# Kernel optimization log

Measured on AMD Instinct MI355X. Metric: run time of the kernel, lower is better.

Reference implementation:

```python
import jax, jax.numpy as jnp
import numpy as np
from jax import lax

N_QUBITS = 8
N_LAYERS = 7


def _conv(x, w, b, stride, pad):
    y = lax.conv_general_dilated(x, w, (stride, stride), [(pad, pad), (pad, pad)],
                                 dimension_numbers=('NCHW', 'OIHW', 'NCHW'))
    return y + b[None, :, None, None]


def _apply_1q(psi, M, q):
    # psi: (B, 2,2,...,2); apply 2x2 real matrix M on qubit q (axis q+1)
    a = q + 1
    pm = jnp.moveaxis(psi, a, 1)
    out = jnp.einsum('ij,bj...->bi...', M, pm)
    return jnp.moveaxis(out, 1, a)


def _apply_cnot(psi, c, t):
    ac, at = c + 1, t + 1
    pm = jnp.moveaxis(psi, (ac, at), (1, 2))
    top = pm[:, 0]
    bot = jnp.flip(pm[:, 1], axis=1)  # flip target when control=1
    pm = jnp.stack([top, bot], axis=1)
    return jnp.moveaxis(pm, (1, 2), (ac, at))


def _quantum(features, qw):
    psi = features / jnp.linalg.norm(features, axis=1, keepdims=True)
    B = psi.shape[0]
    psi = psi.reshape((B,) + (2,) * N_QUBITS)
    for l in range(N_LAYERS):
        for q in range(N_QUBITS):
            th = qw[l, q] / 2.0
            c, s = jnp.cos(th), jnp.sin(th)
            M = jnp.stack([jnp.stack([c, -s]), jnp.stack([s, c])])
            psi = _apply_1q(psi, M, q)
        for q in range(N_QUBITS - 1):
            psi = _apply_cnot(psi, q, q + 1)
    p = psi.reshape(B, 2, -1) ** 2
    return jnp.sum(p[:, 0], axis=1) - jnp.sum(p[:, 1], axis=1)  # <PauliZ(0)>


def setup_inputs() -> dict:
    key = jax.random.key(0)
    ks = jax.random.split(key, 20)
    def g(k, shape, fan_in):
        return jax.random.normal(k, shape, jnp.float32) * (1.0 / np.sqrt(fan_in))
    inp = {
        'x':  jax.random.normal(ks[0], (4096, 1, 64, 64), jnp.float32),
        'w1': g(ks[1], (4, 1, 5, 5), 25), 'b1': jnp.zeros((4,), jnp.float32),
        'w2': g(ks[2], (8, 4, 3, 3), 36), 'b2': jnp.zeros((8,), jnp.float32),
        'w3': g(ks[3], (16, 8, 3, 3), 72), 'b3': jnp.zeros((16,), jnp.float32),
        'wf': g(ks[4], (256, 64), 64), 'bf': jnp.zeros((256,), jnp.float32),
        'qw': jax.random.uniform(ks[5], (7, 8), jnp.float32, 0.0, 2 * np.pi),
        'wc1': g(ks[6], (200, 1), 1),   'bc1': jnp.zeros((200,), jnp.float32),
        'wc2': g(ks[7], (150, 200), 200), 'bc2': jnp.zeros((150,), jnp.float32),
        'wc3': g(ks[8], (100, 150), 150), 'bc3': jnp.zeros((100,), jnp.float32),
        'wc4': g(ks[9], (50, 100), 100),  'bc4': jnp.zeros((50,), jnp.float32),
        'wc5': g(ks[10], (1, 50), 50),    'bc5': jnp.zeros((1,), jnp.float32),
    }
    return inp


def reference(x, w1, b1, w2, b2, w3, b3, wf, bf, qw,
              wc1, bc1, wc2, bc2, wc3, bc3, wc4, bc4, wc5, bc5):
    # CNN feature extractor (dropout = identity at inference)
    h = jax.nn.relu(_conv(x, w1, b1, 2, 2))   # (B,4,32,32)
    h = jax.nn.relu(_conv(h, w2, b2, 2, 1))   # (B,8,16,16)
    h = jax.nn.relu(_conv(h, w3, b3, 1, 1))   # (B,16,16,16)
    B = h.shape[0]
    # AdaptiveAvgPool2d(2): 16x16 -> 2x2 via 8x8 non-overlapping means
    h = h.reshape(B, 16, 2, 8, 2, 8).mean(axis=(3, 5))  # (B,16,2,2)
    h = h.reshape(B, 64)
    feats = jax.nn.relu(h @ wf.T + bf)        # (B,256)
    # F.normalize(p=2, dim=1)
    feats = feats / jnp.maximum(jnp.linalg.norm(feats, axis=1, keepdims=True), 1e-12)
    # Batched 8-qubit statevector simulation (replaces per-sample Python loop)
    q = _quantum(feats, qw)[:, None]          # (B,1)
    # MLP classifier
    h = jax.nn.relu(q @ wc1.T + bc1)
    h = jax.nn.relu(h @ wc2.T + bc2)
    h = jax.nn.relu(h @ wc3.T + bc3)
    h = jax.nn.relu(h @ wc4.T + bc4)
    return jax.nn.sigmoid(h @ wc5.T + bc5)    # (B,1)
```

## Files before the change

### kernel.cpp

```cpp
#include <hip/hip_runtime.h>
#include <math.h>

typedef float v2f __attribute__((ext_vector_type(2)));
#define FMA2(a, b, c) __builtin_elementwise_fma((a), (b), (c))

__global__ __launch_bounds__(256, 8)
void convpool_kernel(const float* __restrict__ x,
                     const float* __restrict__ w1, const float* __restrict__ b1,
                     const float* __restrict__ w2, const float* __restrict__ b2,
                     const float* __restrict__ w3, const float* __restrict__ b3,
                     float* __restrict__ poolout)
{
    __shared__ __align__(16) float arena[4648];
    const int tid  = threadIdx.x;
    const int b    = blockIdx.x;
    const int lane = tid & 63;

    float wstage[7];
    #pragma unroll
    for (int j = 0; j < 7; j++) {
        const int s  = tid + 256 * j;
        const int oc = s / 100;
        const int r  = s - oc * 100;
        const int ic = r / 12;
        const int k  = r - ic * 12;
        wstage[j] = (s < 1600 && r < 96 && k < 9) ? w3[oc * 72 + ic * 9 + k] : 0.f;
    }
    const float bstage = (tid < 16) ? b3[tid] : 0.f;

    if (tid < 40) arena[4608 + tid] = 0.f;

    {
        const float* xb = x + (size_t)b * 4096;
        const int oh  = tid >> 3;
        const int ow  = tid & 7;
        const int ow0 = ow * 4;
        const int c0  = ow0 * 2 - 2;
        const bool cmL = (ow == 0);
        const bool cmR = (ow == 7);
        v2f a01[4], a23[4];
        #pragma unroll
        for (int oc = 0; oc < 4; oc++) {
            const float bv = b1[oc];
            a01[oc] = (v2f){bv, bv};
            a23[oc] = (v2f){bv, bv};
        }
        #pragma unroll
        for (int kh = 0; kh < 5; kh++) {
            const int ih = oh * 2 - 2 + kh;
            if (ih >= 0 && ih < 64) {
                const float* row = xb + ih * 64;
                float colv[11];
                {
                    float v0 = row[cmL ? 0 : c0];
                    float v1 = row[cmL ? 0 : c0 + 1];
                    float vA = row[cmR ? 63 : c0 + 10];
                    colv[0]  = cmL ? 0.f : v0;
                    colv[1]  = cmL ? 0.f : v1;
                    colv[10] = cmR ? 0.f : vA;
                }
                {
                    const float4 m0 = *(const float4*)(row + c0 + 2);
                    const float4 m1 = *(const float4*)(row + c0 + 6);
                    colv[2] = m0.x; colv[3] = m0.y; colv[4] = m0.z; colv[5] = m0.w;
                    colv[6] = m1.x; colv[7] = m1.y; colv[8] = m1.z; colv[9] = m1.w;
                }
                #pragma unroll
                for (int kw = 0; kw < 5; kw++) {
                    const v2f c01 = {colv[kw],     colv[kw + 2]};
                    const v2f c23 = {colv[kw + 4], colv[kw + 6]};
                    #pragma unroll
                    for (int oc = 0; oc < 4; oc++) {
                        const float wv = w1[oc * 25 + kh * 5 + kw];
                        const v2f ws = {wv, wv};
                        a01[oc] = FMA2(c01, ws, a01[oc]);
                        a23[oc] = FMA2(c23, ws, a23[oc]);
                    }
                }
            }
        }
        const int bsw1 = (oh >> 1) & 1;
        #pragma unroll
        for (int oc = 0; oc < 4; oc++) {
            float4 v;
            v.x = fmaxf(a01[oc].x, 0.f); v.y = fmaxf(a01[oc].y, 0.f);
            v.z = fmaxf(a23[oc].x, 0.f); v.w = fmaxf(a23[oc].y, 0.f);
            *(float4*)(arena + oc * 1152 + oh * 36 + ((ow ^ bsw1) << 2)) = v;
        }
    }
    __syncthreads();

    v2f rA01, rA23, rB01, rB23;
    {
        const int oc0 = __builtin_amdgcn_readfirstlane(tid >> 6);
        const int oh  = lane >> 2;
        const int w   = lane & 3;
        {
            const float ba = b2[oc0], bb = b2[oc0 + 4];
            rA01 = (v2f){ba, ba}; rA23 = (v2f){ba, ba};
            rB01 = (v2f){bb, bb}; rB23 = (v2f){bb, bb};
        }
        #pragma unroll
        for (int ic = 0; ic < 4; ic++) {
            const float* base = arena + ic * 1152;
            #pragma unroll
            for (int kh = 0; kh < 3; kh++) {
                const int r2 = 2 * oh + kh - 1;
                const bool zr = (kh == 0) && (oh == 0);
                const int rc = zr ? 0 : r2;
                const int bsw = (rc >> 1) & 1;
                const float* row = zr ? (arena + 4608) : (base + rc * 36);
                const float4 qA = *(const float4*)(row + (((2 * w)     ^ bsw) << 2));
                const float4 qB = *(const float4*)(row + (((2 * w + 1) ^ bsw) << 2));
                const int sblk = (w == 0) ? bsw : ((2 * w - 1) ^ bsw);
                const float sv = row[(sblk << 2) + 3];
                float colv[9];
                colv[0] = (w == 0) ? 0.f : sv;
                colv[1] = qA.x; colv[2] = qA.y; colv[3] = qA.z; colv[4] = qA.w;
                colv[5] = qB.x; colv[6] = qB.y; colv[7] = qB.z; colv[8] = qB.w;
                #pragma unroll
                for (int kw = 0; kw < 3; kw++) {
                    const v2f c01 = {colv[kw],     colv[kw + 2]};
                    const v2f c23 = {colv[kw + 4], colv[kw + 6]};
                    const float wa = w2[((oc0    ) * 4 + ic) * 9 + kh * 3 + kw];
                    const float wb = w2[((oc0 + 4) * 4 + ic) * 9 + kh * 3 + kw];
                    const v2f was = {wa, wa}, wbs = {wb, wb};
                    rA01 = FMA2(c01, was, rA01);
                    rA23 = FMA2(c23, was, rA23);
                    rB01 = FMA2(c01, wbs, rB01);
                    rB23 = FMA2(c23, wbs, rB23);
                }
            }
        }
    }
    __syncthreads();

    for (int i = tid; i < 544; i += 256) {
        const int ch = i / 68, j = i - ch * 68;
        if (j < 18)      arena[ch * 360 + j] = 0.f;
        else if (j < 36) arena[ch * 360 + 17 * 20 + (j - 18)] = 0.f;
        else if (j < 52) arena[ch * 360 + (j - 35) * 20] = 0.f;
        else             arena[ch * 360 + (j - 51) * 20 + 17] = 0.f;
    }
    {
        const int oc0 = __builtin_amdgcn_readfirstlane(tid >> 6);
        const int oh  = lane >> 2, ow0 = (lane & 3) * 4;
        float* oA = arena + oc0 * 360       + (oh + 1) * 20 + ow0 + 1;
        float* oB = arena + (oc0 + 4) * 360 + (oh + 1) * 20 + ow0 + 1;
        oA[0] = fmaxf(rA01.x, 0.f); oA[1] = fmaxf(rA01.y, 0.f);
        oA[2] = fmaxf(rA23.x, 0.f); oA[3] = fmaxf(rA23.y, 0.f);
        oB[0] = fmaxf(rB01.x, 0.f); oB[1] = fmaxf(rB01.y, 0.f);
        oB[2] = fmaxf(rB23.x, 0.f); oB[3] = fmaxf(rB23.y, 0.f);
    }
    #pragma unroll
    for (int j = 0; j < 7; j++) {
        const int s = tid + 256 * j;
        if (s < 1600) arena[2880 + s] = wstage[j];
    }
    if (tid < 16) arena[4480 + tid] = bstage;
    __syncthreads();

    {
        const float* w3s = arena + 2880;
        const int oc = tid >> 4, s = tid & 15;
        const int tr = (s >> 2) * 4, tc = (s & 3) * 4;
        v2f acc2[4][2];
        const float bv = w3s[1600 + oc];
        #pragma unroll
        for (int r = 0; r < 4; r++) {
            acc2[r][0] = (v2f){bv, bv};
            acc2[r][1] = (v2f){bv, bv};
        }
        #pragma unroll
        for (int ic = 0; ic < 8; ic++) {
            const float* xc = arena + ic * 360;
            const float4 wv0 = *(const float4*)(w3s + oc * 100 + ic * 12);
            const float4 wv1 = *(const float4*)(w3s + oc * 100 + ic * 12 + 4);
            const float  wv8 = w3s[oc * 100 + ic * 12 + 8];
            const float wv[9] = {wv0.x, wv0.y, wv0.z, wv0.w, wv1.x, wv1.y, wv1.z, wv1.w, wv8};
            #pragma unroll
            for (int j = 0; j < 6; j++) {
                const float* rp = xc + (tr + j) * 20 + tc;
                const float4 qa = *(const float4*)(rp);
                const float4 qb = *(const float4*)(rp + 4);
                const v2f e0 = {qa.x, qa.y};
                const v2f o0 = {qa.y, qa.z};
                const v2f e1 = {qa.z, qa.w};
                const v2f o1 = {qa.w, qb.x};
                const v2f e2 = {qb.x, qb.y};
                #pragma unroll
                for (int r = 0; r < 4; r++) {
                    const int kh = j - r;
                    if (kh >= 0 && kh < 3) {
                        const v2f w0s = {wv[kh * 3 + 0], wv[kh * 3 + 0]};
                        const v2f w1s = {wv[kh * 3 + 1], wv[kh * 3 + 1]};
                        const v2f w2s = {wv[kh * 3 + 2], wv[kh * 3 + 2]};
                        acc2[r][0] = FMA2(e0, w0s, acc2[r][0]);
                        acc2[r][0] = FMA2(o0, w1s, acc2[r][0]);
                        acc2[r][0] = FMA2(e1, w2s, acc2[r][0]);
                        acc2[r][1] = FMA2(e1, w0s, acc2[r][1]);
                        acc2[r][1] = FMA2(o1, w1s, acc2[r][1]);
                        acc2[r][1] = FMA2(e2, w2s, acc2[r][1]);
                    }
                }
            }
        }
        float ps = 0.f;
        #pragma unroll
        for (int r = 0; r < 4; r++) {
            ps += fmaxf(acc2[r][0].x, 0.f);
            ps += fmaxf(acc2[r][0].y, 0.f);
            ps += fmaxf(acc2[r][1].x, 0.f);
            ps += fmaxf(acc2[r][1].y, 0.f);
        }
        ps += __shfl_xor(ps, 1, 64);
        ps += __shfl_xor(ps, 4, 64);
        if ((s & 5) == 0) {
            const int ii = s >> 3, jj = (s >> 1) & 1;
            poolout[b * 64 + oc * 4 + ii * 2 + jj] = ps * (1.f / 64.f);
        }
    }
}

__global__ __launch_bounds__(256)
void head_kernel(const float* __restrict__ poolin,
                 const float* __restrict__ wf, const float* __restrict__ bf,
                 const float* __restrict__ qw,
                 const float* __restrict__ wc1, const float* __restrict__ bc1,
                 const float* __restrict__ wc2, const float* __restrict__ bc2,
                 const float* __restrict__ wc3, const float* __restrict__ bc3,
                 const float* __restrict__ wc4, const float* __restrict__ bc4,
                 const float* __restrict__ wc5, const float* __restrict__ bc5,
                 float* __restrict__ out)
{
    __shared__ __align__(16) float pool_s[256];
    __shared__ __align__(16) float feats[1024];
    __shared__ __align__(16) float h1[800];
    __shared__ __align__(16) float h2[600];
    __shared__ __align__(16) float h3[400];
    __shared__ __align__(16) float h4[200];
    __shared__ float zbuf[4];
    __shared__ float csc[56], css[56];

    const int tid  = threadIdx.x;
    const int blk  = blockIdx.x;
    const int lane = tid & 63;
    const int wv   = tid >> 6;

    pool_s[tid] = poolin[(size_t)blk * 256 + tid];
    if (tid < 56) {
        float th = qw[tid] * 0.5f;
        csc[tid] = cosf(th);
        css[tid] = sinf(th);
    }
    __syncthreads();

    {
        float acc[4];
        const float bv = bf[tid];
        #pragma unroll
        for (int e = 0; e < 4; e++) acc[e] = bv;
        const float4* wr = (const float4*)(wf + tid * 64);
        #pragma unroll
        for (int kc = 0; kc < 4; kc++) {
            float4 w0 = wr[kc * 4 + 0], w1_ = wr[kc * 4 + 1], w2_ = wr[kc * 4 + 2], w3_ = wr[kc * 4 + 3];
            #pragma unroll
            for (int e = 0; e < 4; e++) {
                const float4* pp = (const float4*)(pool_s + e * 64 + kc * 16);
                float4 p0 = pp[0], p1 = pp[1], p2 = pp[2], p3 = pp[3];
                float a = acc[e];
                a = fmaf(w0.x, p0.x, a); a = fmaf(w0.y, p0.y, a); a = fmaf(w0.z, p0.z, a); a = fmaf(w0.w, p0.w, a);
                a = fmaf(w1_.x, p1.x, a); a = fmaf(w1_.y, p1.y, a); a = fmaf(w1_.z, p1.z, a); a = fmaf(w1_.w, p1.w, a);
                a = fmaf(w2_.x, p2.x, a); a = fmaf(w2_.y, p2.y, a); a = fmaf(w2_.z, p2.z, a); a = fmaf(w2_.w, p2.w, a);
                a = fmaf(w3_.x, p3.x, a); a = fmaf(w3_.y, p3.y, a); a = fmaf(w3_.z, p3.z, a); a = fmaf(w3_.w, p3.w, a);
                acc[e] = a;
            }
        }
        #pragma unroll
        for (int e = 0; e < 4; e++) feats[e * 256 + tid] = fmaxf(acc[e], 0.f);
    }
    __syncthreads();

    {
        const float* base = feats + wv * 256;
        float v0 = base[lane], v1 = base[64 + lane];
        float v2 = base[128 + lane], v3 = base[192 + lane];
        float ssq = v0 * v0 + v1 * v1 + v2 * v2 + v3 * v3;
        #pragma unroll
        for (int off = 1; off < 64; off <<= 1) ssq += __shfl_xor(ssq, off, 64);
        const float inv = 1.0f / fmaxf(sqrtf(ssq), 1e-12f);
        v0 *= inv; v1 *= inv; v2 *= inv; v3 *= inv;

        for (int l = 0; l < 7; l++) {
            {
                float c = csc[l * 8 + 0], s = css[l * 8 + 0];
                float n0 = c * v0 - s * v2, n2 = s * v0 + c * v2;
                float n1 = c * v1 - s * v3, n3 = s * v1 + c * v3;
                float c1 = csc[l * 8 + 1], s1 = css[l * 8 + 1];
                v0 = c1 * n0 - s1 * n1; v1 = s1 * n0 + c1 * n1;
                v2 = c1 * n2 - s1 * n3; v3 = s1 * n2 + c1 * n3;
            }
            #pragma unroll
            for (int q = 2; q < 8; q++) {
                const int m = 1 << (7 - q);
                const float c = csc[l * 8 + q], s = css[l * 8 + q];
                const float sgn = (lane & m) ? s : -s;
                float t0 = __shfl_xor(v0, m, 64);
                float t1 = __shfl_xor(v1, m, 64);
                float t2 = __shfl_xor(v2, m, 64);
                float t3 = __shfl_xor(v3, m, 64);
                v0 = fmaf(sgn, t0, c * v0);
                v1 = fmaf(sgn, t1, c * v1);
                v2 = fmaf(sgn, t2, c * v2);
                v3 = fmaf(sgn, t3, c * v3);
            }
            { float t = v2; v2 = v3; v3 = t; }
            v1 = __shfl_xor(v1, 32, 64);
            v3 = __shfl_xor(v3, 32, 64);
            #pragma unroll
            for (int q = 2; q < 7; q++) {
                const int mc = 1 << (7 - q), mt = 1 << (6 - q);
                float t0 = __shfl_xor(v0, mt, 64);
                float t1 = __shfl_xor(v1, mt, 64);
                float t2 = __shfl_xor(v2, mt, 64);
                float t3 = __shfl_xor(v3, mt, 64);
                if (lane & mc) { v0 = t0; v1 = t1; v2 = t2; v3 = t3; }
            }
        }
        float m0 = v0 * v0 + v1 * v1 - v2 * v2 - v3 * v3;
        #pragma unroll
        for (int off = 1; off < 64; off <<= 1) m0 += __shfl_xor(m0, off, 64);
        if (lane == 0) zbuf[wv] = m0;
    }
    __syncthreads();

    if (tid < 200) {
        const float w = wc1[tid], bv = bc1[tid];
        #pragma unroll
        for (int e = 0; e < 4; e++) h1[e * 200 + tid] = fmaxf(fmaf(zbuf[e], w, bv), 0.f);
    }
    __syncthreads();
    if (tid < 150) {
        float acc[4];
        const float bv = bc2[tid];
        #pragma unroll
        for (int e = 0; e < 4; e++) acc[e] = bv;
        const float4* wr = (const float4*)(wc2 + tid * 200);
        for (int kc = 0; kc < 25; kc++) {
            float4 wa = wr[2 * kc], wb = wr[2 * kc + 1];
            #pragma unroll
            for (int e = 0; e < 4; e++) {
                const float4* hp = (const float4*)(h1 + e * 200) + 2 * kc;
                float4 ha = hp[0], hb = hp[1];
                float a = acc[e];
                a = fmaf(wa.x, ha.x, a); a = fmaf(wa.y, ha.y, a); a = fmaf(wa.z, ha.z, a); a = fmaf(wa.w, ha.w, a);
                a = fmaf(wb.x, hb.x, a); a = fmaf(wb.y, hb.y, a); a = fmaf(wb.z, hb.z, a); a = fmaf(wb.w, hb.w, a);
                acc[e] = a;
            }
        }
        #pragma unroll
        for (int e = 0; e < 4; e++) h2[e * 150 + tid] = fmaxf(acc[e], 0.f);
    }
    __syncthreads();
    if (tid < 100) {
        float acc[4];
        const float bv = bc3[tid];
        #pragma unroll
        for (int e = 0; e < 4; e++) acc[e] = bv;
        const float2* wr = (const float2*)(wc3 + tid * 150);
        for (int k = 0; k < 75; k++) {
            float2 wa = wr[k];
            #pragma unroll
            for (int e = 0; e < 4; e++) {
                float2 hv = ((const float2*)(h2 + e * 150))[k];
                acc[e] = fmaf(wa.x, hv.x, fmaf(wa.y, hv.y, acc[e]));
            }
        }
        #pragma unroll
        for (int e = 0; e < 4; e++) h3[e * 100 + tid] = fmaxf(acc[e], 0.f);
    }
    __syncthreads();
    if (tid < 50) {
        float acc[4];
        const float bv = bc4[tid];
        #pragma unroll
        for (int e = 0; e < 4; e++) acc[e] = bv;
        const float4* wr = (const float4*)(wc4 + tid * 100);
        for (int kc = 0; kc < 25; kc++) {
            float4 wa = wr[kc];
            #pragma unroll
            for (int e = 0; e < 4; e++) {
                float4 hv = ((const float4*)(h3 + e * 100))[kc];
                float a = acc[e];
                a = fmaf(wa.x, hv.x, a); a = fmaf(wa.y, hv.y, a);
                a = fmaf(wa.z, hv.z, a); a = fmaf(wa.w, hv.w, a);
                acc[e] = a;
            }
        }
        #pragma unroll
        for (int e = 0; e < 4; e++) h4[e * 50 + tid] = fmaxf(acc[e], 0.f);
    }
    __syncthreads();
    if (tid < 4) {
        float acc = bc5[0];
        const float2* wr = (const float2*)wc5;
        #pragma unroll
        for (int k = 0; k < 25; k++) {
            float2 wa = wr[k];
            float2 hv = ((const float2*)(h4 + tid * 50))[k];
            acc = fmaf(wa.x, hv.x, fmaf(wa.y, hv.y, acc));
        }
        out[blk * 4 + tid] = 1.0f / (1.0f + expf(-acc));
    }
}

extern "C" void kernel_launch(void* const* d_in, const int* in_sizes, int n_in,
                              void* d_out, int out_size, void* d_ws, size_t ws_size,
                              hipStream_t stream) {
    const float* x   = (const float*)d_in[0];
    const float* w1  = (const float*)d_in[1];
    const float* b1  = (const float*)d_in[2];
    const float* w2  = (const float*)d_in[3];
    const float* b2  = (const float*)d_in[4];
    const float* w3  = (const float*)d_in[5];
    const float* b3  = (const float*)d_in[6];
    const float* wf  = (const float*)d_in[7];
    const float* bf  = (const float*)d_in[8];
    const float* qw  = (const float*)d_in[9];
    const float* wc1 = (const float*)d_in[10];
    const float* bc1 = (const float*)d_in[11];
    const float* wc2 = (const float*)d_in[12];
    const float* bc2 = (const float*)d_in[13];
    const float* wc3 = (const float*)d_in[14];
    const float* bc3 = (const float*)d_in[15];
    const float* wc4 = (const float*)d_in[16];
    const float* bc4 = (const float*)d_in[17];
    const float* wc5 = (const float*)d_in[18];
    const float* bc5 = (const float*)d_in[19];
    float* out = (float*)d_out;

    float* poolbuf = (float*)d_ws;

    convpool_kernel<<<4096, 256, 0, stream>>>(x, w1, b1, w2, b2, w3, b3, poolbuf);
    head_kernel<<<1024, 256, 0, stream>>>(poolbuf, wf, bf, qw,
                                          wc1, bc1, wc2, bc2, wc3, bc3,
                                          wc4, bc4, wc5, bc5, out);
}
```

Before: 215.6 us.

## Fuse head MLP and quantum simulation into conv kernel per sample

Merges the separate head kernel into the conv/pool kernel so each block carries its pooled features through the linear layer, the statevector simulation and the MLP in shared memory, writing only the final output. This removes the second launch and the workspace round trip of pooled features. In exchange, the head weights are no longer amortised over four samples per block, and the serial head stages lengthen every conv block with many threads idle.

```diff
diff --git a/kernel.cpp b/kernel.cpp
--- a/kernel.cpp
+++ b/kernel.cpp
@@ -9,9 +9,18 @@
                      const float* __restrict__ w1, const float* __restrict__ b1,
                      const float* __restrict__ w2, const float* __restrict__ b2,
                      const float* __restrict__ w3, const float* __restrict__ b3,
-                     float* __restrict__ poolout)
+                     const float* __restrict__ wf, const float* __restrict__ bf,
+                     const float* __restrict__ qw,
+                     const float* __restrict__ wc1, const float* __restrict__ bc1,
+                     const float* __restrict__ wc2, const float* __restrict__ bc2,
+                     const float* __restrict__ wc3, const float* __restrict__ bc3,
+                     const float* __restrict__ wc4, const float* __restrict__ bc4,
+                     const float* __restrict__ wc5, const float* __restrict__ bc5,
+                     float* __restrict__ out)
 {
     __shared__ __align__(16) float arena[4648];
+    __shared__ __align__(16) float csc[56], css[56];
+
     const int tid  = threadIdx.x;
     const int b    = blockIdx.x;
     const int lane = tid & 63;
@@ -27,6 +36,12 @@
         wstage[j] = (s < 1600 && r < 96 && k < 9) ? w3[oc * 72 + ic * 9 + k] : 0.f;
     }
     const float bstage = (tid < 16) ? b3[tid] : 0.f;
+
+    if (tid < 56) {
+        const float th = qw[tid] * 0.5f;
+        csc[tid] = cosf(th);
+        css[tid] = sinf(th);
+    }
 
     if (tid < 40) arena[4608 + tid] = 0.f;
 
@@ -217,74 +232,31 @@
         ps += __shfl_xor(ps, 4, 64);
         if ((s & 5) == 0) {
             const int ii = s >> 3, jj = (s >> 1) & 1;
-            poolout[b * 64 + oc * 4 + ii * 2 + jj] = ps * (1.f / 64.f);
-        }
-    }
-}
-
-__global__ __launch_bounds__(256)
-void head_kernel(const float* __restrict__ poolin,
-                 const float* __restrict__ wf, const float* __restrict__ bf,
-                 const float* __restrict__ qw,
-                 const float* __restrict__ wc1, const float* __restrict__ bc1,
-                 const float* __restrict__ wc2, const float* __restrict__ bc2,
-                 const float* __restrict__ wc3, const float* __restrict__ bc3,
-                 const float* __restrict__ wc4, const float* __restrict__ bc4,
-                 const float* __restrict__ wc5, const float* __restrict__ bc5,
-                 float* __restrict__ out)
-{
-    __shared__ __align__(16) float pool_s[256];
-    __shared__ __align__(16) float feats[1024];
-    __shared__ __align__(16) float h1[800];
-    __shared__ __align__(16) float h2[600];
-    __shared__ __align__(16) float h3[400];
-    __shared__ __align__(16) float h4[200];
-    __shared__ float zbuf[4];
-    __shared__ float csc[56], css[56];
-
-    const int tid  = threadIdx.x;
-    const int blk  = blockIdx.x;
-    const int lane = tid & 63;
-    const int wv   = tid >> 6;
-
-    pool_s[tid] = poolin[(size_t)blk * 256 + tid];
-    if (tid < 56) {
-        float th = qw[tid] * 0.5f;
-        csc[tid] = cosf(th);
-        css[tid] = sinf(th);
-    }
-    __syncthreads();
-
-    {
-        float acc[4];
-        const float bv = bf[tid];
-        #pragma unroll
-        for (int e = 0; e < 4; e++) acc[e] = bv;
+            arena[4496 + oc * 4 + ii * 2 + jj] = ps * (1.f / 64.f);
+        }
+    }
+    __syncthreads();
+
+    {
+        const float* pool = arena + 4496;
+        float a = bf[tid];
         const float4* wr = (const float4*)(wf + tid * 64);
-        #pragma unroll
-        for (int kc = 0; kc < 4; kc++) {
-            float4 w0 = wr[kc * 4 + 0], w1_ = wr[kc * 4 + 1], w2_ = wr[kc * 4 + 2], w3_ = wr[kc * 4 + 3];
-            #pragma unroll
-            for (int e = 0; e < 4; e++) {
-                const float4* pp = (const float4*)(pool_s + e * 64 + kc * 16);
-                float4 p0 = pp[0], p1 = pp[1], p2 = pp[2], p3 = pp[3];
-                float a = acc[e];
-                a = fmaf(w0.x, p0.x, a); a = fmaf(w0.y, p0.y, a); a = fmaf(w0.z, p0.z, a); a = fmaf(w0.w, p0.w, a);
-                a = fmaf(w1_.x, p1.x, a); a = fmaf(w1_.y, p1.y, a); a = fmaf(w1_.z, p1.z, a); a = fmaf(w1_.w, p1.w, a);
-                a = fmaf(w2_.x, p2.x, a); a = fmaf(w2_.y, p2.y, a); a = fmaf(w2_.z, p2.z, a); a = fmaf(w2_.w, p2.w, a);
-                a = fmaf(w3_.x, p3.x, a); a = fmaf(w3_.y, p3.y, a); a = fmaf(w3_.z, p3.z, a); a = fmaf(w3_.w, p3.w, a);
-                acc[e] = a;
-            }
-        }
-        #pragma unroll
-        for (int e = 0; e < 4; e++) feats[e * 256 + tid] = fmaxf(acc[e], 0.f);
-    }
-    __syncthreads();
-
-    {
-        const float* base = feats + wv * 256;
-        float v0 = base[lane], v1 = base[64 + lane];
-        float v2 = base[128 + lane], v3 = base[192 + lane];
+        const float4* pp = (const float4*)pool;
+        #pragma unroll
+        for (int kc = 0; kc < 16; kc++) {
+            const float4 w = wr[kc];
+            const float4 p = pp[kc];
+            a = fmaf(w.x, p.x, a); a = fmaf(w.y, p.y, a);
+            a = fmaf(w.z, p.z, a); a = fmaf(w.w, p.w, a);
+        }
+        __syncthreads();
+        arena[tid] = fmaxf(a, 0.f);
+    }
+    __syncthreads();
+
+    if (tid < 64) {
+        float v0 = arena[lane], v1 = arena[64 + lane];
+        float v2 = arena[128 + lane], v3 = arena[192 + lane];
         float ssq = v0 * v0 + v1 * v1 + v2 * v2 + v3 * v3;
         #pragma unroll
         for (int off = 1; off < 64; off <<= 1) ssq += __shfl_xor(ssq, off, 64);
@@ -330,87 +302,63 @@
         float m0 = v0 * v0 + v1 * v1 - v2 * v2 - v3 * v3;
         #pragma unroll
         for (int off = 1; off < 64; off <<= 1) m0 += __shfl_xor(m0, off, 64);
-        if (lane == 0) zbuf[wv] = m0;
+        if (lane == 0) arena[760] = m0;
     }
     __syncthreads();
 
     if (tid < 200) {
-        const float w = wc1[tid], bv = bc1[tid];
-        #pragma unroll
-        for (int e = 0; e < 4; e++) h1[e * 200 + tid] = fmaxf(fmaf(zbuf[e], w, bv), 0.f);
+        arena[256 + tid] = fmaxf(fmaf(arena[760], wc1[tid], bc1[tid]), 0.f);
     }
     __syncthreads();
     if (tid < 150) {
-        float acc[4];
-        const float bv = bc2[tid];
-        #pragma unroll
-        for (int e = 0; e < 4; e++) acc[e] = bv;
+        float a = bc2[tid];
         const float4* wr = (const float4*)(wc2 + tid * 200);
+        const float4* hp = (const float4*)(arena + 256);
         for (int kc = 0; kc < 25; kc++) {
-            float4 wa = wr[2 * kc], wb = wr[2 * kc + 1];
-            #pragma unroll
-            for (int e = 0; e < 4; e++) {
-                const float4* hp = (const float4*)(h1 + e * 200) + 2 * kc;
-                float4 ha = hp[0], hb = hp[1];
-                float a = acc[e];
-                a = fmaf(wa.x, ha.x, a); a = fmaf(wa.y, ha.y, a); a = fmaf(wa.z, ha.z, a); a = fmaf(wa.w, ha.w, a);
-                a = fmaf(wb.x, hb.x, a); a = fmaf(wb.y, hb.y, a); a = fmaf(wb.z, hb.z, a); a = fmaf(wb.w, hb.w, a);
-                acc[e] = a;
-            }
-        }
-        #pragma unroll
-        for (int e = 0; e < 4; e++) h2[e * 150 + tid] = fmaxf(acc[e], 0.f);
+            const float4 wa = wr[2 * kc], wb = wr[2 * kc + 1];
+            const float4 ha = hp[2 * kc], hb = hp[2 * kc + 1];
+            a = fmaf(wa.x, ha.x, a); a = fmaf(wa.y, ha.y, a); a = fmaf(wa.z, ha.z, a); a = fmaf(wa.w, ha.w, a);
+            a = fmaf(wb.x, hb.x, a); a = fmaf(wb.y, hb.y, a); a = fmaf(wb.z, hb.z, a); a = fmaf(wb.w, hb.w, a);
+        }
+        arena[456 + tid] = fmaxf(a, 0.f);
     }
     __syncthreads();
     if (tid < 100) {
-        float acc[4];
-        const float bv = bc3[tid];
-        #pragma unroll
-        for (int e = 0; e < 4; e++) acc[e] = bv;
+        float a = bc3[tid];
         const float2* wr = (const float2*)(wc3 + tid * 150);
+        const float2* hp = (const float2*)(arena + 456);
         for (int k = 0; k < 75; k++) {
-            float2 wa = wr[k];
-            #pragma unroll
-            for (int e = 0; e < 4; e++) {
-                float2 hv = ((const float2*)(h2 + e * 150))[k];
-                acc[e] = fmaf(wa.x, hv.x, fmaf(wa.y, hv.y, acc[e]));
-            }
-        }
-        #pragma unroll
-        for (int e = 0; e < 4; e++) h3[e * 100 + tid] = fmaxf(acc[e], 0.f);
+            const float2 wa = wr[k];
+            const float2 hv = hp[k];
+            a = fmaf(wa.x, hv.x, fmaf(wa.y, hv.y, a));
+        }
+        arena[608 + tid] = fmaxf(a, 0.f);
     }
     __syncthreads();
     if (tid < 50) {
-        float acc[4];
-        const float bv = bc4[tid];
-        #pragma unroll
-        for (int e = 0; e < 4; e++) acc[e] = bv;
+        float a = bc4[tid];
         const float4* wr = (const float4*)(wc4 + tid * 100);
+        const float4* hp = (const float4*)(arena + 608);
         for (int kc = 0; kc < 25; kc++) {
-            float4 wa = wr[kc];
-            #pragma unroll
-            for (int e = 0; e < 4; e++) {
-                float4 hv = ((const float4*)(h3 + e * 100))[kc];
-                float a = acc[e];
-                a = fmaf(wa.x, hv.x, a); a = fmaf(wa.y, hv.y, a);
-                a = fmaf(wa.z, hv.z, a); a = fmaf(wa.w, hv.w, a);
-                acc[e] = a;
-            }
-        }
-        #pragma unroll
-        for (int e = 0; e < 4; e++) h4[e * 50 + tid] = fmaxf(acc[e], 0.f);
-    }
-    __syncthreads();
-    if (tid < 4) {
-        float acc = bc5[0];
+            const float4 wa = wr[kc];
+            const float4 hv = hp[kc];
+            a = fmaf(wa.x, hv.x, a); a = fmaf(wa.y, hv.y, a);
+            a = fmaf(wa.z, hv.z, a); a = fmaf(wa.w, hv.w, a);
+        }
+        arena[708 + tid] = fmaxf(a, 0.f);
+    }
+    __syncthreads();
+    if (tid == 0) {
+        float a = bc5[0];
         const float2* wr = (const float2*)wc5;
+        const float2* hp = (const float2*)(arena + 708);
         #pragma unroll
         for (int k = 0; k < 25; k++) {
-            float2 wa = wr[k];
-            float2 hv = ((const float2*)(h4 + tid * 50))[k];
-            acc = fmaf(wa.x, hv.x, fmaf(wa.y, hv.y, acc));
-        }
-        out[blk * 4 + tid] = 1.0f / (1.0f + expf(-acc));
+            const float2 wa = wr[k];
+            const float2 hv = hp[k];
+            a = fmaf(wa.x, hv.x, fmaf(wa.y, hv.y, a));
+        }
+        out[b] = 1.0f / (1.0f + expf(-a));
     }
 }
 
@@ -439,10 +387,8 @@
     const float* bc5 = (const float*)d_in[19];
     float* out = (float*)d_out;
 
-    float* poolbuf = (float*)d_ws;
-
-    convpool_kernel<<<4096, 256, 0, stream>>>(x, w1, b1, w2, b2, w3, b3, poolbuf);
-    head_kernel<<<1024, 256, 0, stream>>>(poolbuf, wf, bf, qw,
-                                          wc1, bc1, wc2, bc2, wc3, bc3,
-                                          wc4, bc4, wc5, bc5, out);
+    convpool_kernel<<<4096, 256, 0, stream>>>(x, w1, b1, w2, b2, w3, b3,
+                                              wf, bf, qw,
+                                              wc1, bc1, wc2, bc2, wc3, bc3,
+                                              wc4, bc4, wc5, bc5, out);
 }
```

Result: slower. 258.8 us (+20.1%).
